# Kernel optimization log

Measured on AMD Instinct MI355X. Metric: run time of the kernel, lower is better.

Reference implementation:

```python
import jax, jax.numpy as jnp
import numpy as np

# Constants matching init_kwargs
PC_MIN_X, PC_MIN_Y = -70.4, -40.0
VX, VY = 0.1, 0.1
RADII = (0.4, 0.8)
NSAMPLE = 16
EPS = 1e-5

B, K, N = 2, 2048, 16384
C_BEV, H_BEV, W_BEV = 256, 100, 176


def setup_inputs() -> dict:
    key = jax.random.key(0)
    ks = jax.random.split(key, 16)
    u = lambda k, s: jax.random.uniform(k, s, jnp.float32)
    kp = jnp.stack([
        u(ks[0], (B, K)) * 136.0 - 68.0,
        u(ks[1], (B, K)) * 76.0 - 38.0,
        u(ks[2], (B, K)) * 2.5 - 2.0,   # z in (-2.0, 0.5) -> kpt_mask all True
    ], axis=-1)
    pts = jnp.stack([
        u(ks[3], (B, N)) * 140.0 - 70.0,
        u(ks[4], (B, N)) * 80.0 - 40.0,
        u(ks[5], (B, N)) * 4.0 - 3.0,
    ], axis=-1)
    r = lambda k, s: jax.random.normal(k, s, jnp.float32)
    s01 = lambda k, s: r(k, s) * 0.1
    return {
        "keypoints": kp,
        "points_xyz": pts,
        "points_feat": r(ks[6], (B, N, 1)),
        "spatial_features": r(ks[7], (B, C_BEV, H_BEV, W_BEV)),
        "bev_stride": 8,
        "W0_s0": s01(ks[8], (16, 4)), "g0_s0": jnp.ones(16), "b0_s0": jnp.zeros(16),
        "W1_s0": s01(ks[9], (16, 16)), "g1_s0": jnp.ones(16), "b1_s0": jnp.zeros(16),
        "W0_s1": s01(ks[10], (16, 4)), "g0_s1": jnp.ones(16), "b0_s1": jnp.zeros(16),
        "W1_s1": s01(ks[11], (32, 16)), "g1_s1": jnp.ones(32), "b1_s1": jnp.zeros(32),
        "Wf": s01(ks[12], (128, 304)), "gf": jnp.ones(128), "bf": jnp.zeros(128),
    }


def _batchnorm(x, g, b, axes):
    m = x.mean(axes, keepdims=True)
    v = x.var(axes, keepdims=True)
    return (x - m) * jax.lax.rsqrt(v + EPS) * g + b


def _ball_group(dist2, xyz_b, feat_b, kp_b, radius, ns):
    """pcdet ball_query: first ns in-radius neighbors (index order), pad by first idx."""
    Kq, Np = dist2.shape
    within = dist2 < radius * radius                      # (K, N)
    order = jnp.cumsum(within, axis=1) - 1                # slot for each point
    valid = within & (order < ns)
    pos = jnp.where(valid, order, ns)                     # invalid -> overflow slot
    idx = jnp.zeros((Kq, ns + 1), jnp.int32)
    idx = idx.at[jnp.arange(Kq)[:, None], pos].set(
        jnp.broadcast_to(jnp.arange(Np, dtype=jnp.int32)[None, :], (Kq, Np)))
    idx = idx[:, :ns]
    cnt = within.sum(axis=1)
    slot_ok = jnp.arange(ns)[None, :] < cnt[:, None]
    idx = jnp.where(slot_ok, idx, idx[:, :1])             # replicate first found idx
    empty = cnt == 0
    grouped_xyz = xyz_b[idx] - kp_b[:, None, :]           # (K, ns, 3)
    grouped = jnp.concatenate([grouped_xyz, feat_b[idx]], axis=-1)  # (K, ns, 3+C)
    grouped = jnp.where(empty[:, None, None], 0.0, grouped)
    return grouped, empty


def _group_both_scales(xyz_b, feat_b, kp_b):
    # pairwise dist computed ONCE, shared across both radii
    dist2 = jnp.sum((kp_b[:, None, :] - xyz_b[None, :, :]) ** 2, axis=-1)  # (K, N)
    g0, e0 = _ball_group(dist2, xyz_b, feat_b, kp_b, RADII[0], NSAMPLE)
    g1, e1 = _ball_group(dist2, xyz_b, feat_b, kp_b, RADII[1], NSAMPLE)
    return g0, e0, g1, e1


def _shared_mlp_pool(grouped, empty, layers):
    x = grouped                                            # (B, K, ns, Cin)
    for (W, g, b) in layers:
        x = jnp.einsum('bknc,oc->bkno', x, W)
        x = _batchnorm(x, g, b, axes=(0, 1, 2))            # BN2d over stacked M*ns
        x = jax.nn.relu(x)
    pooled = x.max(axis=2)                                 # max over ns -> (B, K, Cout)
    return jnp.where(empty[:, :, None], 0.0, pooled)


def _bev_interp(bev, kp, stride):
    # bev: (B, C, H, W); kp: (B, K, 3)
    im = jnp.transpose(bev, (0, 2, 3, 1))                  # (B, H, W, C)
    x = (kp[..., 0] - PC_MIN_X) / VX / stride
    y = (kp[..., 1] - PC_MIN_Y) / VY / stride
    Hh, Ww = im.shape[1], im.shape[2]
    x0 = jnp.clip(jnp.floor(x).astype(jnp.int32), 0, Ww - 1)
    x1 = jnp.clip(jnp.floor(x).astype(jnp.int32) + 1, 0, Ww - 1)
    y0 = jnp.clip(jnp.floor(y).astype(jnp.int32), 0, Hh - 1)
    y1 = jnp.clip(jnp.floor(y).astype(jnp.int32) + 1, 0, Hh - 1)
    bidx = jnp.arange(im.shape[0])[:, None]
    Ia, Ib = im[bidx, y0, x0], im[bidx, y1, x0]
    Ic, Id = im[bidx, y0, x1], im[bidx, y1, x1]
    x0f, x1f = x0.astype(x.dtype), x1.astype(x.dtype)
    y0f, y1f = y0.astype(y.dtype), y1.astype(y.dtype)
    wa = ((x1f - x) * (y1f - y))[..., None]
    wb = ((x1f - x) * (y - y0f))[..., None]
    wc = ((x - x0f) * (y1f - y))[..., None]
    wd = ((x - x0f) * (y - y0f))[..., None]
    return Ia * wa + Ib * wb + Ic * wc + Id * wd           # (B, K, C)


def reference(keypoints, points_xyz, points_feat, spatial_features, bev_stride,
              W0_s0, g0_s0, b0_s0, W1_s0, g1_s0, b1_s0,
              W0_s1, g0_s1, b0_s1, W1_s1, g1_s1, b1_s1,
              Wf, gf, bf):
    Bb, Kk, _ = keypoints.shape
    # BEV bilinear interpolation
    bev_feat = _bev_interp(spatial_features, keypoints, bev_stride)  # (B, K, C_bev)
    # per-batch ball-query grouping (vmapped over batch)
    g0, e0, g1, e1 = jax.vmap(_group_both_scales)(points_xyz, points_feat, keypoints)
    p0 = _shared_mlp_pool(g0, e0, [(W0_s0, g0_s0, b0_s0), (W1_s0, g1_s0, b1_s0)])
    p1 = _shared_mlp_pool(g1, e1, [(W0_s1, g0_s1, b0_s1), (W1_s1, g1_s1, b1_s1)])
    pooled = jnp.concatenate([p0, p1], axis=-1)            # (B, K, 48)
    feats = jnp.concatenate([bev_feat, pooled], axis=-1).reshape(Bb * Kk, -1)  # (M, 304)
    # vsa_point_feature_fusion: Linear(no bias) + BN1d(train) + ReLU
    fused = feats @ Wf.T
    fused = jax.nn.relu(_batchnorm(fused, gf, bf, axes=(0,)))
    return fused                                           # (B*K, 128)
```

## Files before the change

### kernel.cpp

```cpp
#include <hip/hip_runtime.h>
#include <hip/hip_bf16.h>

#define NB    2
#define NK    2048
#define NPTS  16384
#define NBK   4096
#define MSAMP 65536.0f
#define MROW  4096.0f

__global__ __launch_bounds__(256) void mega_kernel(
    const float* __restrict__ kp, const float* __restrict__ pts,
    const float* __restrict__ pfeat, const float* __restrict__ bev,
    const int* __restrict__ stridep,
    float* __restrict__ g0buf, float* __restrict__ g1buf,
    int* __restrict__ cnt, float* __restrict__ part0,
    float* __restrict__ feats)
{
  __shared__ __align__(16) float4 sxyzf[1024];
  __shared__ float slots[4][2][16][4];
  __shared__ float bred[4][28];
  const int t = threadIdx.x;

  if (blockIdx.x >= 1024) {
    const int bk = blockIdx.x - 1024;
    const int c  = t;
    const int b  = bk >> 11;
    const float st = (float)(*stridep);
    const float x = (kp[bk*3+0] - (-70.4f)) / 0.1f / st;
    const float y = (kp[bk*3+1] - (-40.0f)) / 0.1f / st;
    const int xf = (int)floorf(x), yf = (int)floorf(y);
    const int x0 = min(max(xf, 0), 175), x1 = min(max(xf + 1, 0), 175);
    const int y0 = min(max(yf, 0), 99),  y1 = min(max(yf + 1, 0), 99);
    const float x0f = (float)x0, x1f = (float)x1, y0f = (float)y0, y1f = (float)y1;
    const float wa = (x1f - x) * (y1f - y);
    const float wb = (x1f - x) * (y - y0f);
    const float wc = (x - x0f) * (y1f - y);
    const float wd = (x - x0f) * (y - y0f);
    const size_t base = ((size_t)b * 256 + c) * 17600;
    const float Ia = bev[base + y0 * 176 + x0];
    const float Ib = bev[base + y1 * 176 + x0];
    const float Ic = bev[base + y0 * 176 + x1];
    const float Id = bev[base + y1 * 176 + x1];
    feats[(size_t)bk * 304 + c] = Ia * wa + Ib * wb + Ic * wc + Id * wd;
    return;
  }

  const int gb = blockIdx.x;
  const int wave = t >> 6;
  const int lane = t & 63;
  const int bk = gb * 4 + wave;
  const int b  = gb >> 9;
  const float kx = kp[bk*3+0];
  const float ky = kp[bk*3+1];
  const float kz = kp[bk*3+2];
  const float* px = pts   + (size_t)b * NPTS * 3;
  const float* pf = pfeat + (size_t)b * NPTS;
  int c0 = 0, c1 = 0;
  bool done = false;
  const unsigned long long below = (1ull << lane) - 1ull;

  for (int tile = 0; tile < 16; tile++) {
    __syncthreads();
    {
      const float4* px4 = (const float4*)px + tile * 768;
      const float4 a = px4[3*t], bb4 = px4[3*t+1], cc = px4[3*t+2];
      const float4 f4 = ((const float4*)pf)[tile * 256 + t];
      sxyzf[4*t+0] = make_float4(a.x, a.y, a.z, f4.x);
      sxyzf[4*t+1] = make_float4(a.w, bb4.x, bb4.y, f4.y);
      sxyzf[4*t+2] = make_float4(bb4.z, bb4.w, cc.x, f4.z);
      sxyzf[4*t+3] = make_float4(cc.y, cc.z, cc.w, f4.w);
    }
    __syncthreads();
    if (!done) {
      for (int inner = 0; inner < 16; inner++) {
        const float4 P = sxyzf[inner * 64 + lane];
        const float dx = P.x - kx, dy = P.y - ky, dz = P.z - kz;
        const float d2 = dx*dx + dy*dy + dz*dz;
        const bool w0 = d2 < 0.16f;
        const bool w1 = d2 < 0.64f;
        const unsigned long long m1 = __ballot(w1);
        if (m1) {
          const unsigned long long m0 = __ballot(w0);
          const int o0 = c0 + __popcll(m0 & below);
          if (w0 && o0 < 16) {
            slots[wave][0][o0][0] = dx; slots[wave][0][o0][1] = dy;
            slots[wave][0][o0][2] = dz; slots[wave][0][o0][3] = P.w;
          }
          const int o1 = c1 + __popcll(m1 & below);
          if (w1 && o1 < 16) {
            slots[wave][1][o1][0] = dx; slots[wave][1][o1][1] = dy;
            slots[wave][1][o1][2] = dz; slots[wave][1][o1][3] = P.w;
          }
          c0 += __popcll(m0);
          c1 += __popcll(m1);
          if (c0 >= 16) { done = true; break; }
        }
      }
    }
  }
  __syncthreads();

  if (lane < 32) {
    const int s  = (lane >> 4) & 1;
    const int sl = lane & 15;
    const int cs = s ? c1 : c0;
    if (cs == 0) {
      slots[wave][s][sl][0] = 0.f; slots[wave][s][sl][1] = 0.f;
      slots[wave][s][sl][2] = 0.f; slots[wave][s][sl][3] = 0.f;
    } else if (sl >= cs) {
      slots[wave][s][sl][0] = slots[wave][s][0][0];
      slots[wave][s][sl][1] = slots[wave][s][0][1];
      slots[wave][s][sl][2] = slots[wave][s][0][2];
      slots[wave][s][sl][3] = slots[wave][s][0][3];
    }
  }

  g0buf[(size_t)bk * 64 + lane] = slots[wave][0][lane >> 2][lane & 3];
  g1buf[(size_t)bk * 64 + lane] = slots[wave][1][lane >> 2][lane & 3];
  if (lane == 0) { cnt[bk] = c0; cnt[NBK + bk] = c1; }

  float v[14];
  {
    float x0 = 0.f, x1 = 0.f, x2 = 0.f, x3 = 0.f;
    if (lane < 32) {
      const int s  = (lane >> 4) & 1;
      const int sl = lane & 15;
      x0 = slots[wave][s][sl][0]; x1 = slots[wave][s][sl][1];
      x2 = slots[wave][s][sl][2]; x3 = slots[wave][s][sl][3];
    }
    v[0] = x0; v[1] = x1; v[2] = x2; v[3] = x3;
    v[4] = x0*x0; v[5] = x0*x1; v[6]  = x0*x2; v[7]  = x0*x3;
    v[8] = x1*x1; v[9] = x1*x2; v[10] = x1*x3;
    v[11] = x2*x2; v[12] = x2*x3; v[13] = x3*x3;
  }
  #pragma unroll
  for (int d = 1; d < 16; d <<= 1) {
    #pragma unroll
    for (int i = 0; i < 14; i++) v[i] += __shfl_xor(v[i], d);
  }
  if (lane == 0 || lane == 16) {
    float* dst = &bred[wave][(lane >> 4) * 14];
    #pragma unroll
    for (int i = 0; i < 14; i++) dst[i] = v[i];
  }
  __syncthreads();
  if (t < 28) {
    part0[gb * 28 + t] = bred[0][t] + bred[1][t] + bred[2][t] + bred[3][t];
  }
}

__device__ __forceinline__ void bn0_params(
    int t, const float* S0, const float* sW0a, const float* sW0b,
    const float* gm0s0, const float* bt0s0,
    const float* gm0s1, const float* bt0s1, float* sP)
{
  if (t < 32) {
    const int s = t >> 4, c = t & 15;
    const float* W  = s ? sW0b : sW0a;
    const float* G  = s ? gm0s1 : gm0s0;
    const float* Bt = s ? bt0s1 : bt0s0;
    const float* Sx = S0 + s * 14;
    const float w0 = W[c*4+0], w1 = W[c*4+1];
    const float w2 = W[c*4+2], w3 = W[c*4+3];
    const float inv = 1.0f / MSAMP;
    const float mean = (w0*Sx[0] + w1*Sx[1] + w2*Sx[2] + w3*Sx[3]) * inv;
    float e2 = w0*w0*Sx[4] + 2.f*w0*w1*Sx[5] + 2.f*w0*w2*Sx[6] + 2.f*w0*w3*Sx[7]
             + w1*w1*Sx[8] + 2.f*w1*w2*Sx[9] + 2.f*w1*w3*Sx[10]
             + w2*w2*Sx[11] + 2.f*w2*w3*Sx[12] + w3*w3*Sx[13];
    e2 *= inv;
    const float var = e2 - mean * mean;
    const float A = G[c] / sqrtf(var + 1e-5f);
    sP[s*32 + c]      = A;
    sP[s*32 + 16 + c] = Bt[c] - mean * A;
  }
}

__global__ __launch_bounds__(256) void stats1_kernel(
    const float* __restrict__ g0buf, const float* __restrict__ g1buf,
    const float* __restrict__ part0,
    const float* __restrict__ W0s0, const float* __restrict__ gm0s0, const float* __restrict__ bt0s0,
    const float* __restrict__ W0s1, const float* __restrict__ gm0s1, const float* __restrict__ bt0s1,
    const float* __restrict__ W1s0, const float* __restrict__ W1s1,
    float* __restrict__ part1)
{
  __shared__ float sW0a[64], sW0b[64], sW1a[256], sW1b[512], sP[64];
  __shared__ float tmp0[8][28], S0[28];
  __shared__ float red[16][96];
  const int t = threadIdx.x;
  if (t < 64) { sW0a[t] = W0s0[t]; sW0b[t] = W0s1[t]; }
  sW1a[t]       = W1s0[t];
  sW1b[t]       = W1s1[t];
  sW1b[t + 256] = W1s1[t + 256];
  for (int i = t; i < 16 * 96; i += 256) ((float*)red)[i] = 0.f;
  if (t < 224) {
    const int seg = t / 28, col = t % 28;
    float s = 0.f;
    for (int r = seg * 128; r < seg * 128 + 128; r++) s += part0[r * 28 + col];
    tmp0[seg][col] = s;
  }
  __syncthreads();
  if (t < 28) {
    float s = 0.f;
    #pragma unroll
    for (int g = 0; g < 8; g++) s += tmp0[g][t];
    S0[t] = s;
  }
  __syncthreads();
  bn0_params(t, S0, sW0a, sW0b, gm0s0, bt0s0, gm0s1, bt0s1, sP);
  __syncthreads();

  const int slot = blockIdx.x * 256 + t;
  const int wave = t >> 6, lane = t & 63;
  const int grp  = (wave << 2) | (lane >> 4);
  const bool leader = (lane & 15) == 0;

  float a1[16];
  {
    const float4 x = *(const float4*)(g0buf + (size_t)slot * 4);
    #pragma unroll
    for (int c = 0; c < 16; c++) {
      const float h = sW0a[c*4+0]*x.x + sW0a[c*4+1]*x.y + sW0a[c*4+2]*x.z + sW0a[c*4+3]*x.w;
      a1[c] = fmaxf(fmaf(sP[c], h, sP[16+c]), 0.f);
    }
    #pragma unroll
    for (int o = 0; o < 16; o++) {
      float h2 = 0.f;
      #pragma unroll
      for (int c = 0; c < 16; c++) h2 = fmaf(sW1a[o*16+c], a1[c], h2);
      float s = h2, q = h2 * h2;
      #pragma unroll
      for (int d = 1; d < 16; d <<= 1) { s += __shfl_xor(s, d); q += __shfl_xor(q, d); }
      if (leader) { red[grp][o] += s; red[grp][16+o] += q; }
    }
  }
  {
    const float4 x = *(const float4*)(g1buf + (size_t)slot * 4);
    #pragma unroll
    for (int c = 0; c < 16; c++) {
      const float h = sW0b[c*4+0]*x.x + sW0b[c*4+1]*x.y + sW0b[c*4+2]*x.z + sW0b[c*4+3]*x.w;
      a1[c] = fmaxf(fmaf(sP[32+c], h, sP[48+c]), 0.f);
    }
    #pragma unroll
    for (int o = 0; o < 32; o++) {
      float h2 = 0.f;
      #pragma unroll
      for (int c = 0; c < 16; c++) h2 = fmaf(sW1b[o*16+c], a1[c], h2);
      float s = h2, q = h2 * h2;
      #pragma unroll
      for (int d = 1; d < 16; d <<= 1) { s += __shfl_xor(s, d); q += __shfl_xor(q, d); }
      if (leader) { red[grp][32+o] += s; red[grp][64+o] += q; }
    }
  }
  __syncthreads();
  if (t < 96) {
    float s = 0.f;
    #pragma unroll
    for (int g = 0; g < 16; g++) s += red[g][t];
    part1[blockIdx.x * 96 + t] = s;
  }
}

__global__ __launch_bounds__(256) void poolgemm_kernel(
    const float* __restrict__ g0buf, const float* __restrict__ g1buf,
    const int* __restrict__ cnt,
    const float* __restrict__ part0, const float* __restrict__ part1,
    const float* __restrict__ W0s0, const float* __restrict__ gm0s0, const float* __restrict__ bt0s0,
    const float* __restrict__ W0s1, const float* __restrict__ gm0s1, const float* __restrict__ bt0s1,
    const float* __restrict__ W1s0, const float* __restrict__ gm1s0, const float* __restrict__ bt1s0,
    const float* __restrict__ W1s1, const float* __restrict__ gm1s1, const float* __restrict__ bt1s1,
    const float* __restrict__ feats, const float* __restrict__ Wf,
    float* __restrict__ fused, float* __restrict__ part2)
{
  __shared__ float sW0a[64], sW0b[64], sW1a[256], sW1b[512], sP[160];
  __shared__ float tmp0[8][28], S0[28];
  __shared__ float tmp1[2][96], S1[96];
  __shared__ __align__(16) float sF[16 * 304];
  const int t = threadIdx.x;
  const int bk0 = blockIdx.x * 16;

  for (int i = t; i < 4096; i += 256) {
    const int row = i >> 8, col = i & 255;
    sF[row * 304 + col] = feats[(size_t)(bk0 + row) * 304 + col];
  }
  if (t < 64)  { sW0a[t] = W0s0[t]; sW0b[t] = W0s1[t]; }
  sW1a[t]       = W1s0[t];
  sW1b[t]       = W1s1[t];
  sW1b[t + 256] = W1s1[t + 256];
  if (t < 224) {
    const int seg = t / 28, col = t % 28;
    float s = 0.f;
    for (int r = seg * 128; r < seg * 128 + 128; r++) s += part0[r * 28 + col];
    tmp0[seg][col] = s;
  }
  __syncthreads();
  if (t < 28) {
    float s = 0.f;
    #pragma unroll
    for (int g = 0; g < 8; g++) s += tmp0[g][t];
    S0[t] = s;
  }
  if (t >= 32 && t < 224) {
    const int tt = t - 32;
    const int seg = tt / 96, col = tt % 96;
    float s = 0.f;
    for (int r = seg * 128; r < seg * 128 + 128; r++) s += part1[r * 96 + col];
    tmp1[seg][col] = s;
  }
  __syncthreads();
  bn0_params(t, S0, sW0a, sW0b, gm0s0, bt0s0, gm0s1, bt0s1, sP);
  if (t >= 64 && t < 160) {
    const int c = t - 64;
    S1[c] = tmp1[0][c] + tmp1[1][c];
  }
  __syncthreads();
  if (t < 48) {
    float sum, sq, G, Bv; int oA, oB;
    if (t < 16) { sum = S1[t];    sq = S1[16+t]; G = gm1s0[t]; Bv = bt1s0[t]; oA = 64+t;  oB = 80+t; }
    else { const int c = t - 16; sum = S1[32+c]; sq = S1[64+c]; G = gm1s1[c]; Bv = bt1s1[c]; oA = 96+c; oB = 128+c; }
    const float mean = sum / MSAMP;
    const float var  = sq / MSAMP - mean * mean;
    const float A = G / sqrtf(var + 1e-5f);
    sP[oA] = A;
    sP[oB] = Bv - mean * A;
  }
  __syncthreads();

  {
    const int lkp = t >> 4, slot = t & 15;
    const int bk = bk0 + lkp;
    const size_t si = (size_t)bk * 16 + slot;
    float a1[16], a2s0[16], a2s1[32];
    {
      const float4 x = *(const float4*)(g0buf + si * 4);
      #pragma unroll
      for (int c = 0; c < 16; c++) {
        const float h = sW0a[c*4+0]*x.x + sW0a[c*4+1]*x.y + sW0a[c*4+2]*x.z + sW0a[c*4+3]*x.w;
        a1[c] = fmaxf(fmaf(sP[c], h, sP[16+c]), 0.f);
      }
      #pragma unroll
      for (int o = 0; o < 16; o++) {
        float h2 = 0.f;
        #pragma unroll
        for (int c = 0; c < 16; c++) h2 = fmaf(sW1a[o*16+c], a1[c], h2);
        a2s0[o] = fmaxf(fmaf(sP[64+o], h2, sP[80+o]), 0.f);
      }
    }
    {
      const float4 x = *(const float4*)(g1buf + si * 4);
      #pragma unroll
      for (int c = 0; c < 16; c++) {
        const float h = sW0b[c*4+0]*x.x + sW0b[c*4+1]*x.y + sW0b[c*4+2]*x.z + sW0b[c*4+3]*x.w;
        a1[c] = fmaxf(fmaf(sP[32+c], h, sP[48+c]), 0.f);
      }
      #pragma unroll
      for (int o = 0; o < 32; o++) {
        float h2 = 0.f;
        #pragma unroll
        for (int c = 0; c < 16; c++) h2 = fmaf(sW1b[o*16+c], a1[c], h2);
        a2s1[o] = fmaxf(fmaf(sP[96+o], h2, sP[128+o]), 0.f);
      }
    }
    #pragma unroll
    for (int d = 1; d < 16; d <<= 1) {
      #pragma unroll
      for (int o = 0; o < 16; o++) a2s0[o] = fmaxf(a2s0[o], __shfl_xor(a2s0[o], d));
      #pragma unroll
      for (int o = 0; o < 32; o++) a2s1[o] = fmaxf(a2s1[o], __shfl_xor(a2s1[o], d));
    }
    if (slot == 0) {
      const int c0 = cnt[bk], c1 = cnt[NBK + bk];
      float* outp = sF + lkp * 304 + 256;
      #pragma unroll
      for (int o = 0; o < 16; o++) outp[o] = c0 ? a2s0[o] : 0.f;
      #pragma unroll
      for (int o = 0; o < 32; o++) outp[16 + o] = c1 ? a2s1[o] : 0.f;
    }
  }
  __syncthreads();

  {
    const int c = t & 127;
    const int rbase = (t >> 7) * 8;
    float acc[8];
    #pragma unroll
    for (int r = 0; r < 8; r++) acc[r] = 0.f;
    const float* wrow = Wf + (size_t)c * 304;
    for (int j4 = 0; j4 < 76; j4++) {
      const float4 w = *(const float4*)(wrow + j4 * 4);
      #pragma unroll
      for (int r = 0; r < 8; r++) {
        const float4 f = *(const float4*)(sF + (rbase + r) * 304 + j4 * 4);
        acc[r] = fmaf(w.x, f.x, acc[r]);
        acc[r] = fmaf(w.y, f.y, acc[r]);
        acc[r] = fmaf(w.z, f.z, acc[r]);
        acc[r] = fmaf(w.w, f.w, acc[r]);
      }
    }
    float s = 0.f, q = 0.f;
    #pragma unroll
    for (int r = 0; r < 8; r++) {
      fused[(size_t)(bk0 + rbase + r) * 128 + c] = acc[r];
      s += acc[r];
      q = fmaf(acc[r], acc[r], q);
    }
    const int prow = blockIdx.x * 2 + (t >> 7);
    part2[prow * 256 + c]       = s;
    part2[prow * 256 + 128 + c] = q;
  }
}

__global__ __launch_bounds__(256) void out_kernel(
    const float* __restrict__ fused, const float* __restrict__ part2,
    const float* __restrict__ gf, const float* __restrict__ bfp,
    float* __restrict__ out)
{
  __shared__ float sA[128], sB[128];
  __shared__ float tmp[2][128];
  const int t = threadIdx.x;
  {
    const int c = t & 127, which = t >> 7;
    float s = 0.f;
    for (int r = 0; r < 512; r++) s += part2[r * 256 + which * 128 + c];
    tmp[which][c] = s;
  }
  __syncthreads();
  if (t < 128) {
    const float mean = tmp[0][t] / MROW;
    const float var  = tmp[1][t] / MROW - mean * mean;
    const float A = gf[t] / sqrtf(var + 1e-5f);
    sA[t] = A;
    sB[t] = bfp[t] - mean * A;
  }
  __syncthreads();
  #pragma unroll
  for (int k = 0; k < 4; k++) {
    const int f4 = blockIdx.x * 1024 + k * 256 + t;
    const int i = f4 * 4;
    const float4 v = *(const float4*)(fused + i);
    const int c = i & 127;
    float4 o;
    o.x = fmaxf(fmaf(v.x, sA[c+0], sB[c+0]), 0.f);
    o.y = fmaxf(fmaf(v.y, sA[c+1], sB[c+1]), 0.f);
    o.z = fmaxf(fmaf(v.z, sA[c+2], sB[c+2]), 0.f);
    o.w = fmaxf(fmaf(v.w, sA[c+3], sB[c+3]), 0.f);
    *(float4*)(out + i) = o;
  }
}

extern "C" void kernel_launch(void* const* d_in, const int* in_sizes, int n_in,
                              void* d_out, int out_size, void* d_ws, size_t ws_size,
                              hipStream_t stream)
{
  const float* kp    = (const float*)d_in[0];
  const float* pts   = (const float*)d_in[1];
  const float* pfeat = (const float*)d_in[2];
  const float* bev   = (const float*)d_in[3];
  const int*   strd  = (const int*)d_in[4];
  const float* W0s0  = (const float*)d_in[5];
  const float* g0s0  = (const float*)d_in[6];
  const float* b0s0  = (const float*)d_in[7];
  const float* W1s0  = (const float*)d_in[8];
  const float* g1s0  = (const float*)d_in[9];
  const float* b1s0  = (const float*)d_in[10];
  const float* W0s1  = (const float*)d_in[11];
  const float* g0s1  = (const float*)d_in[12];
  const float* b0s1  = (const float*)d_in[13];
  const float* W1s1  = (const float*)d_in[14];
  const float* g1s1  = (const float*)d_in[15];
  const float* b1s1  = (const float*)d_in[16];
  const float* Wf    = (const float*)d_in[17];
  const float* gf    = (const float*)d_in[18];
  const float* bfv   = (const float*)d_in[19];

  float* w      = (float*)d_ws;
  float* g0buf  = w;
  float* g1buf  = w + 262144;
  float* feats  = w + 524288;
  float* fused  = w + 1769472;
  float* part0  = w + 2293760;
  float* part1  = w + 2326528;
  float* part2  = w + 2351104;
  int*   cnt    = (int*)(w + 2482176);

  hipLaunchKernelGGL(mega_kernel,  dim3(5120), dim3(256), 0, stream,
                     kp, pts, pfeat, bev, strd, g0buf, g1buf, cnt, part0, feats);
  hipLaunchKernelGGL(stats1_kernel, dim3(256), dim3(256), 0, stream,
                     g0buf, g1buf, part0,
                     W0s0, g0s0, b0s0, W0s1, g0s1, b0s1, W1s0, W1s1, part1);
  hipLaunchKernelGGL(poolgemm_kernel, dim3(256), dim3(256), 0, stream,
                     g0buf, g1buf, cnt, part0, part1,
                     W0s0, g0s0, b0s0, W0s1, g0s1, b0s1,
                     W1s0, g1s0, b1s0, W1s1, g1s1, b1s1,
                     feats, Wf, fused, part2);
  hipLaunchKernelGGL(out_kernel,   dim3(128), dim3(256), 0, stream,
                     fused, part2, gf, bfv, (float*)d_out);
}
```

Before: 224.0 us.

## Process two keypoints per wave in ball query to reuse loaded point tiles

Each wave now handles two keypoints, so every staged tile of points is tested against both, halving the grouping blocks from 1024 to 512 and halving the global point loads. The shared staging switches from an interleaved float4 xyz+feat layout to a plain xyz copy plus a separate feature array, with the feature read only when some lane is in radius. The early exit now waits until both keypoints have filled the small radius, and the partial-stat readers are adjusted to 512 rows. This costs more registers and ballots per iteration, and the strided 3-float shared reads may cause bank conflicts.

```diff
diff --git a/kernel.cpp b/kernel.cpp
--- a/kernel.cpp
+++ b/kernel.cpp
@@ -16,13 +16,14 @@
     int* __restrict__ cnt, float* __restrict__ part0,
     float* __restrict__ feats)
 {
-  __shared__ __align__(16) float4 sxyzf[1024];
-  __shared__ float slots[4][2][16][4];
+  __shared__ float sxyz[3072];
+  __shared__ float sfeat[1024];
+  __shared__ float slots[4][2][2][16][4];
   __shared__ float bred[4][28];
   const int t = threadIdx.x;
 
-  if (blockIdx.x >= 1024) {
-    const int bk = blockIdx.x - 1024;
+  if (blockIdx.x >= 512) {
+    const int bk = blockIdx.x - 512;
     const int c  = t;
     const int b  = bk >> 11;
     const float st = (float)(*stridep);
@@ -48,86 +49,118 @@
   const int gb = blockIdx.x;
   const int wave = t >> 6;
   const int lane = t & 63;
-  const int bk = gb * 4 + wave;
-  const int b  = gb >> 9;
-  const float kx = kp[bk*3+0];
-  const float ky = kp[bk*3+1];
-  const float kz = kp[bk*3+2];
+  const int bkA = gb * 8 + wave * 2;
+  const int bkB = bkA + 1;
+  const int b  = gb >> 8;
+  const float kxA = kp[bkA*3+0], kyA = kp[bkA*3+1], kzA = kp[bkA*3+2];
+  const float kxB = kp[bkB*3+0], kyB = kp[bkB*3+1], kzB = kp[bkB*3+2];
   const float* px = pts   + (size_t)b * NPTS * 3;
   const float* pf = pfeat + (size_t)b * NPTS;
-  int c0 = 0, c1 = 0;
+  int c0A = 0, c1A = 0, c0B = 0, c1B = 0;
   bool done = false;
   const unsigned long long below = (1ull << lane) - 1ull;
 
   for (int tile = 0; tile < 16; tile++) {
     __syncthreads();
     {
-      const float4* px4 = (const float4*)px + tile * 768;
-      const float4 a = px4[3*t], bb4 = px4[3*t+1], cc = px4[3*t+2];
-      const float4 f4 = ((const float4*)pf)[tile * 256 + t];
-      sxyzf[4*t+0] = make_float4(a.x, a.y, a.z, f4.x);
-      sxyzf[4*t+1] = make_float4(a.w, bb4.x, bb4.y, f4.y);
-      sxyzf[4*t+2] = make_float4(bb4.z, bb4.w, cc.x, f4.z);
-      sxyzf[4*t+3] = make_float4(cc.y, cc.z, cc.w, f4.w);
+      const float4* gsrc = (const float4*)(px + tile * 3072);
+      float4* ldst = (float4*)sxyz;
+      ldst[t]       = gsrc[t];
+      ldst[t + 256] = gsrc[t + 256];
+      ldst[t + 512] = gsrc[t + 512];
+      #pragma unroll
+      for (int i = 0; i < 4; i++) sfeat[t + i * 256] = pf[tile * 1024 + t + i * 256];
     }
     __syncthreads();
     if (!done) {
       for (int inner = 0; inner < 16; inner++) {
-        const float4 P = sxyzf[inner * 64 + lane];
-        const float dx = P.x - kx, dy = P.y - ky, dz = P.z - kz;
-        const float d2 = dx*dx + dy*dy + dz*dz;
-        const bool w0 = d2 < 0.16f;
-        const bool w1 = d2 < 0.64f;
-        const unsigned long long m1 = __ballot(w1);
-        if (m1) {
-          const unsigned long long m0 = __ballot(w0);
-          const int o0 = c0 + __popcll(m0 & below);
-          if (w0 && o0 < 16) {
-            slots[wave][0][o0][0] = dx; slots[wave][0][o0][1] = dy;
-            slots[wave][0][o0][2] = dz; slots[wave][0][o0][3] = P.w;
+        const int pp = inner * 64 + lane;
+        const float x = sxyz[pp*3+0];
+        const float y = sxyz[pp*3+1];
+        const float z = sxyz[pp*3+2];
+        const float dxA = x - kxA, dyA = y - kyA, dzA = z - kzA;
+        const float d2A = dxA*dxA + dyA*dyA + dzA*dzA;
+        const float dxB = x - kxB, dyB = y - kyB, dzB = z - kzB;
+        const float d2B = dxB*dxB + dyB*dyB + dzB*dzB;
+        const bool w1a = d2A < 0.64f;
+        const bool w1b = d2B < 0.64f;
+        const unsigned long long m1a = __ballot(w1a);
+        const unsigned long long m1b = __ballot(w1b);
+        if (m1a | m1b) {
+          const bool w0a = d2A < 0.16f;
+          const bool w0b = d2B < 0.16f;
+          const unsigned long long m0a = __ballot(w0a);
+          const unsigned long long m0b = __ballot(w0b);
+          const float f = sfeat[pp];
+          {
+            const int o0 = c0A + __popcll(m0a & below);
+            if (w0a && o0 < 16) {
+              slots[wave][0][0][o0][0] = dxA; slots[wave][0][0][o0][1] = dyA;
+              slots[wave][0][0][o0][2] = dzA; slots[wave][0][0][o0][3] = f;
+            }
+            const int o1 = c1A + __popcll(m1a & below);
+            if (w1a && o1 < 16) {
+              slots[wave][0][1][o1][0] = dxA; slots[wave][0][1][o1][1] = dyA;
+              slots[wave][0][1][o1][2] = dzA; slots[wave][0][1][o1][3] = f;
+            }
+            c0A += __popcll(m0a);
+            c1A += __popcll(m1a);
           }
-          const int o1 = c1 + __popcll(m1 & below);
-          if (w1 && o1 < 16) {
-            slots[wave][1][o1][0] = dx; slots[wave][1][o1][1] = dy;
-            slots[wave][1][o1][2] = dz; slots[wave][1][o1][3] = P.w;
+          {
+            const int o0 = c0B + __popcll(m0b & below);
+            if (w0b && o0 < 16) {
+              slots[wave][1][0][o0][0] = dxB; slots[wave][1][0][o0][1] = dyB;
+              slots[wave][1][0][o0][2] = dzB; slots[wave][1][0][o0][3] = f;
+            }
+            const int o1 = c1B + __popcll(m1b & below);
+            if (w1b && o1 < 16) {
+              slots[wave][1][1][o1][0] = dxB; slots[wave][1][1][o1][1] = dyB;
+              slots[wave][1][1][o1][2] = dzB; slots[wave][1][1][o1][3] = f;
+            }
+            c0B += __popcll(m0b);
+            c1B += __popcll(m1b);
           }
-          c0 += __popcll(m0);
-          c1 += __popcll(m1);
-          if (c0 >= 16) { done = true; break; }
+          if (c0A >= 16 && c0B >= 16) { done = true; break; }
         }
       }
     }
   }
   __syncthreads();
 
-  if (lane < 32) {
-    const int s  = (lane >> 4) & 1;
-    const int sl = lane & 15;
-    const int cs = s ? c1 : c0;
+  {
+    const int kpid = lane >> 5;
+    const int s    = (lane >> 4) & 1;
+    const int sl   = lane & 15;
+    const int cs = kpid ? (s ? c1B : c0B) : (s ? c1A : c0A);
     if (cs == 0) {
-      slots[wave][s][sl][0] = 0.f; slots[wave][s][sl][1] = 0.f;
-      slots[wave][s][sl][2] = 0.f; slots[wave][s][sl][3] = 0.f;
+      slots[wave][kpid][s][sl][0] = 0.f; slots[wave][kpid][s][sl][1] = 0.f;
+      slots[wave][kpid][s][sl][2] = 0.f; slots[wave][kpid][s][sl][3] = 0.f;
     } else if (sl >= cs) {
-      slots[wave][s][sl][0] = slots[wave][s][0][0];
-      slots[wave][s][sl][1] = slots[wave][s][0][1];
-      slots[wave][s][sl][2] = slots[wave][s][0][2];
-      slots[wave][s][sl][3] = slots[wave][s][0][3];
-    }
-  }
-
-  g0buf[(size_t)bk * 64 + lane] = slots[wave][0][lane >> 2][lane & 3];
-  g1buf[(size_t)bk * 64 + lane] = slots[wave][1][lane >> 2][lane & 3];
-  if (lane == 0) { cnt[bk] = c0; cnt[NBK + bk] = c1; }
+      slots[wave][kpid][s][sl][0] = slots[wave][kpid][s][0][0];
+      slots[wave][kpid][s][sl][1] = slots[wave][kpid][s][0][1];
+      slots[wave][kpid][s][sl][2] = slots[wave][kpid][s][0][2];
+      slots[wave][kpid][s][sl][3] = slots[wave][kpid][s][0][3];
+    }
+  }
+
+  g0buf[(size_t)bkA * 64 + lane] = slots[wave][0][0][lane >> 2][lane & 3];
+  g1buf[(size_t)bkA * 64 + lane] = slots[wave][0][1][lane >> 2][lane & 3];
+  g0buf[(size_t)bkB * 64 + lane] = slots[wave][1][0][lane >> 2][lane & 3];
+  g1buf[(size_t)bkB * 64 + lane] = slots[wave][1][1][lane >> 2][lane & 3];
+  if (lane == 0) {
+    cnt[bkA] = c0A; cnt[NBK + bkA] = c1A;
+    cnt[bkB] = c0B; cnt[NBK + bkB] = c1B;
+  }
 
   float v[14];
   {
-    float x0 = 0.f, x1 = 0.f, x2 = 0.f, x3 = 0.f;
-    if (lane < 32) {
-      const int s  = (lane >> 4) & 1;
-      const int sl = lane & 15;
-      x0 = slots[wave][s][sl][0]; x1 = slots[wave][s][sl][1];
-      x2 = slots[wave][s][sl][2]; x3 = slots[wave][s][sl][3];
-    }
+    const int kpid = lane >> 5;
+    const int s    = (lane >> 4) & 1;
+    const int sl   = lane & 15;
+    const float x0 = slots[wave][kpid][s][sl][0];
+    const float x1 = slots[wave][kpid][s][sl][1];
+    const float x2 = slots[wave][kpid][s][sl][2];
+    const float x3 = slots[wave][kpid][s][sl][3];
     v[0] = x0; v[1] = x1; v[2] = x2; v[3] = x3;
     v[4] = x0*x0; v[5] = x0*x1; v[6]  = x0*x2; v[7]  = x0*x3;
     v[8] = x1*x1; v[9] = x1*x2; v[10] = x1*x3;
@@ -138,6 +171,8 @@
     #pragma unroll
     for (int i = 0; i < 14; i++) v[i] += __shfl_xor(v[i], d);
   }
+  #pragma unroll
+  for (int i = 0; i < 14; i++) v[i] += __shfl_xor(v[i], 32);
   if (lane == 0 || lane == 16) {
     float* dst = &bred[wave][(lane >> 4) * 14];
     #pragma unroll
@@ -195,7 +230,7 @@
   if (t < 224) {
     const int seg = t / 28, col = t % 28;
     float s = 0.f;
-    for (int r = seg * 128; r < seg * 128 + 128; r++) s += part0[r * 28 + col];
+    for (int r = seg * 64; r < seg * 64 + 64; r++) s += part0[r * 28 + col];
     tmp0[seg][col] = s;
   }
   __syncthreads();
@@ -289,7 +324,7 @@
   if (t < 224) {
     const int seg = t / 28, col = t % 28;
     float s = 0.f;
-    for (int r = seg * 128; r < seg * 128 + 128; r++) s += part0[r * 28 + col];
+    for (int r = seg * 64; r < seg * 64 + 64; r++) s += part0[r * 28 + col];
     tmp0[seg][col] = s;
   }
   __syncthreads();
@@ -482,7 +517,7 @@
   float* part2  = w + 2351104;
   int*   cnt    = (int*)(w + 2482176);
 
-  hipLaunchKernelGGL(mega_kernel,  dim3(5120), dim3(256), 0, stream,
+  hipLaunchKernelGGL(mega_kernel,  dim3(4608), dim3(256), 0, stream,
                      kp, pts, pfeat, bev, strd, g0buf, g1buf, cnt, part0, feats);
   hipLaunchKernelGGL(stats1_kernel, dim3(256), dim3(256), 0, stream,
                      g0buf, g1buf, part0,
```

Result: faster. 218.5 us (-2.4%).
